# Optimization experiments

Hardware: AMD Instinct MI355X
Metric: run time of the kernel (lower is better)

Reference implementation:

```python
import jax, jax.numpy as jnp
import numpy as np

S = 256      # pair sequence length (multiple of 32 -> no padding needed)
C = 128      # pair hidden dim
H = 4        # n_heads
D = 32       # head_dim
EPS = 1e-5
ENDING = False


def setup_inputs() -> dict:
    key = jax.random.key(0)
    ks = jax.random.split(key, 10)
    s = 0.02
    return {
        "x": jax.random.normal(ks[0], (1, S, S, C), dtype=jnp.float32),
        "ln_w": jnp.ones((C,), dtype=jnp.float32),
        "ln_b": jnp.zeros((C,), dtype=jnp.float32),
        "w_bias": jax.random.normal(ks[1], (H, C), dtype=jnp.float32) * s,   # linear.weight
        "w_q": jax.random.normal(ks[2], (H * D, C), dtype=jnp.float32) * s,  # linear_q.weight
        "w_k": jax.random.normal(ks[3], (H * D, C), dtype=jnp.float32) * s,
        "w_v": jax.random.normal(ks[4], (H * D, C), dtype=jnp.float32) * s,
        "w_g": jax.random.normal(ks[5], (H * D, C), dtype=jnp.float32) * s,  # linear_g.weight
        "w_o": jax.random.normal(ks[6], (C, H * D), dtype=jnp.float32) * s,  # linear_o.weight
    }


def reference(x, ln_w, ln_b, w_bias, w_q, w_k, w_v, w_g, w_o):
    h = x[0]  # [S, S, C]
    if ENDING:
        h = jnp.transpose(h, (1, 0, 2))
    # LayerNorm over channel dim
    mu = jnp.mean(h, axis=-1, keepdims=True)
    var = jnp.mean(jnp.square(h - mu), axis=-1, keepdims=True)
    h = (h - mu) * jax.lax.rsqrt(var + EPS) * ln_w + ln_b

    # pair-derived additive bias: [H, S, S], broadcast over the row (batch) dim
    tri_bias = jnp.einsum("ijc,hc->hij", h, w_bias)

    # per-head Q/K/V: weights are [H*D, C] with head-major rows
    wq = w_q.reshape(H, D, C)
    wk = w_k.reshape(H, D, C)
    wv = w_v.reshape(H, D, C)
    q = jnp.einsum("ijc,hdc->hijd", h, wq)  # [H, S(row), S(seq), D]
    k = jnp.einsum("ijc,hdc->hijd", h, wk)
    v = jnp.einsum("ijc,hdc->hijd", h, wv)

    scale = D ** -0.5
    # scores[h, i, j, k] = scale * q[h,i,j]\cdot k[h,i,k] + bias[h, j, k]
    scores = jnp.einsum("hijd,hikd->hijk", q, k) * scale + tri_bias[:, None, :, :]
    attn = jax.nn.softmax(scores, axis=-1)
    o = jnp.einsum("hijk,hikd->hijd", attn, v)          # [H, S, S, D]
    o = jnp.transpose(o, (1, 2, 0, 3)).reshape(S, S, H * D)

    # sigmoid gating and output projection
    g = jax.nn.sigmoid(jnp.einsum("ijc,ec->ije", h, w_g))
    out = jnp.einsum("ije,ce->ijc", o * g, w_o)          # [S, S, C]
    if ENDING:
        out = jnp.transpose(out, (1, 0, 2))
    return out[None]  # [1, S, S, C]
```

## Files before the change

kernel.cpp:

```cpp
#include <hip/hip_runtime.h>
#include <hip/hip_bf16.h>
#include <math.h>

#define SS 256
#define CC 128
#define NH 4
#define HD 32
#define M_TOT (SS*SS)
#define HEAD_STRIDE (M_TOT*HD)
#define PSTR 72
#define SCALE 0.17677669529663687f
#define QSCL 0.25507602861154995f
#define LOG2E 1.4426950408889634f

typedef short short8 __attribute__((ext_vector_type(8)));
typedef float f32x4 __attribute__((ext_vector_type(4)));
typedef unsigned short ushort_t;

static __device__ __forceinline__ unsigned int f2bf(float f) {
  unsigned int u = __builtin_bit_cast(unsigned int, f);
  u += 0x7fffu + ((u >> 16) & 1u);
  return u >> 16;
}
static __device__ __forceinline__ float bf2f(unsigned short b) {
  unsigned int u = ((unsigned int)b) << 16;
  return __builtin_bit_cast(float, u);
}

static __device__ __forceinline__ void async_copy16(const void* g, void* l) {
  __builtin_amdgcn_global_load_lds(
      (const __attribute__((address_space(1))) unsigned int*)g,
      (__attribute__((address_space(3))) unsigned int*)l, 16, 0, 0);
}

__global__ __launch_bounds__(256) void pack_w(
    const float* __restrict__ wq, const float* __restrict__ wk,
    const float* __restrict__ wv, const float* __restrict__ wg,
    const float* __restrict__ wb, const float* __restrict__ wo,
    ushort_t* __restrict__ wcomb, ushort_t* __restrict__ wbias,
    ushort_t* __restrict__ wobf) {
  int idx = blockIdx.x*256 + threadIdx.x;
  if (idx >= 656*128) return;
  int n = idx >> 7, kk = idx & 127;
  if (n < 512) {
    float val;
    if (n < 128)      val = wq[n*128 + kk];
    else if (n < 256) val = wk[(n-128)*128 + kk];
    else if (n < 384) val = wv[(n-256)*128 + kk];
    else              val = wg[(n-384)*128 + kk];
    wcomb[idx] = (ushort_t)f2bf(val);
  } else if (n < 528) {
    int r = n - 512;
    wbias[r*128 + kk] = (r < NH) ? (ushort_t)f2bf(wb[r*128 + kk] * LOG2E) : (ushort_t)0;
  } else {
    int r = n - 528;
    wobf[r*128 + kk] = (ushort_t)f2bf(wo[r*128 + kk]);
  }
}

__global__ __launch_bounds__(256, 2) void fused_proj(
    const float* __restrict__ x, const float* __restrict__ ln_w,
    const float* __restrict__ ln_b, const ushort_t* __restrict__ wcomb,
    const ushort_t* __restrict__ wbias,
    ushort_t* __restrict__ qb, ushort_t* __restrict__ kb,
    ushort_t* __restrict__ vb, ushort_t* __restrict__ gbf,
    float* __restrict__ biasF) {
  __shared__ ushort_t Ash[128*128];
  __shared__ ushort_t Bsh[128*128];
  int mbase = blockIdx.x * 128;
  int tid = threadIdx.x;
  int wvi = tid >> 6, lane = tid & 63;
  int quad = lane >> 4, l15 = lane & 15;
  int lrow4 = lane >> 4;
  int cl = lane & 15;

  #pragma unroll
  for (int t = 0; t < 8; t++) {
    int inst = wvi*8 + t;
    int row = inst*4 + lrow4;
    int gc = cl ^ (row & 7);
    async_copy16(wcomb + (size_t)row*128 + gc*8, Bsh + inst*512);
  }

  {
    int l = tid & 31;
    int rsub = tid >> 5;
    float4 w4 = *(const float4*)&ln_w[l*4];
    float4 b4 = *(const float4*)&ln_b[l*4];
    const float* xb = x + (size_t)(mbase + rsub)*CC + l*4;
    float4 vv[16];
    #pragma unroll
    for (int pass = 0; pass < 16; pass++)
      vv[pass] = *(const float4*)(xb + (size_t)pass*8*CC);
    #pragma unroll
    for (int pass = 0; pass < 16; pass++) {
      int row = pass*8 + rsub;
      float4 v = vv[pass];
      float s  = v.x + v.y + v.z + v.w;
      float s2 = v.x*v.x + v.y*v.y + v.z*v.z + v.w*v.w;
      #pragma unroll
      for (int o = 16; o > 0; o >>= 1) {
        s  += __shfl_xor(s, o);
        s2 += __shfl_xor(s2, o);
      }
      float mu  = s * (1.0f/CC);
      float var = s2 * (1.0f/CC) - mu*mu;
      float r = rsqrtf(var + 1e-5f);
      ushort4 o4;
      o4.x = (ushort_t)f2bf((v.x - mu) * r * w4.x + b4.x);
      o4.y = (ushort_t)f2bf((v.y - mu) * r * w4.y + b4.y);
      o4.z = (ushort_t)f2bf((v.z - mu) * r * w4.z + b4.z);
      o4.w = (ushort_t)f2bf((v.w - mu) * r * w4.w + b4.w);
      int addr = row*128 + (((l >> 1) ^ (row & 7)) << 3) + (l & 1)*4;
      *(ushort4*)&Ash[addr] = o4;
    }
  }
  __syncthreads();

  int wrow = (wvi >> 1) * 64, wcol = (wvi & 1) * 64;
  const f32x4 fz = {0.f,0.f,0.f,0.f};

  short8 Afr[4][4];
  #pragma unroll
  for (int s = 0; s < 4; s++)
    #pragma unroll
    for (int f = 0; f < 4; f++) {
      int ra = wrow + f*16 + l15;
      Afr[s][f] = *(const short8*)&Ash[ra*128 + (((s*4+quad) ^ (ra&7)) << 3)];
    }

  #pragma unroll
  for (int sec = 0; sec < 4; sec++) {
    f32x4 acc[4][4];
    #pragma unroll
    for (int a = 0; a < 4; a++)
      #pragma unroll
      for (int b = 0; b < 4; b++) acc[a][b] = fz;

    #pragma unroll
    for (int s = 0; s < 4; s++) {
      short8 Bf[4];
      #pragma unroll
      for (int f = 0; f < 4; f++) {
        int rb = wcol + f*16 + l15;
        Bf[f] = *(const short8*)&Bsh[rb*128 + (((s*4+quad) ^ (rb&7)) << 3)];
      }
      #pragma unroll
      for (int mi = 0; mi < 4; mi++)
        #pragma unroll
        for (int ni = 0; ni < 4; ni++)
          acc[mi][ni] = __builtin_amdgcn_mfma_f32_16x16x32_bf16(Bf[ni], Afr[s][mi], acc[mi][ni], 0, 0, 0);
    }

    __syncthreads();

    if (sec < 3) {
      #pragma unroll
      for (int t = 0; t < 8; t++) {
        int inst = wvi*8 + t;
        int row = inst*4 + lrow4;
        int gc = cl ^ (row & 7);
        async_copy16(wcomb + (size_t)((sec+1)*128 + row)*128 + gc*8, Bsh + inst*512);
      }
    }

    #pragma unroll
    for (int mi = 0; mi < 4; mi++) {
      int m = mbase + wrow + mi*16 + l15;
      #pragma unroll
      for (int ni = 0; ni < 4; ni++) {
        int n = wcol + ni*16 + quad*4;
        f32x4 v4 = acc[mi][ni];
        if (sec == 0) {
          ushort4 o4;
          o4.x = (ushort_t)f2bf(v4[0] * QSCL);
          o4.y = (ushort_t)f2bf(v4[1] * QSCL);
          o4.z = (ushort_t)f2bf(v4[2] * QSCL);
          o4.w = (ushort_t)f2bf(v4[3] * QSCL);
          *(ushort4*)&qb[(size_t)(n>>5)*HEAD_STRIDE + (size_t)m*HD + (n&31)] = o4;
        } else if (sec == 1) {
          ushort4 o4;
          o4.x = (ushort_t)f2bf(v4[0]);
          o4.y = (ushort_t)f2bf(v4[1]);
          o4.z = (ushort_t)f2bf(v4[2]);
          o4.w = (ushort_t)f2bf(v4[3]);
          *(ushort4*)&kb[(size_t)(n>>5)*HEAD_STRIDE + (size_t)m*HD + (n&31)] = o4;
        } else if (sec == 2) {
          ushort4 o4;
          o4.x = (ushort_t)f2bf(v4[0]);
          o4.y = (ushort_t)f2bf(v4[1]);
          o4.z = (ushort_t)f2bf(v4[2]);
          o4.w = (ushort_t)f2bf(v4[3]);
          *(ushort4*)&vb[(size_t)(n>>5)*HEAD_STRIDE + (size_t)m*HD + (n&31)] = o4;
        } else {
          ushort4 o4;
          o4.x = (ushort_t)f2bf(1.0f/(1.0f + __expf(-v4[0])));
          o4.y = (ushort_t)f2bf(1.0f/(1.0f + __expf(-v4[1])));
          o4.z = (ushort_t)f2bf(1.0f/(1.0f + __expf(-v4[2])));
          o4.w = (ushort_t)f2bf(1.0f/(1.0f + __expf(-v4[3])));
          *(ushort4*)&gbf[(size_t)m*CC + n] = o4;
        }
      }
    }

    if (sec == 0) {
      short8 wbF[4];
      #pragma unroll
      for (int s = 0; s < 4; s++)
        wbF[s] = *(const short8*)&wbias[l15*128 + s*32 + quad*8];
      #pragma unroll
      for (int t2 = 0; t2 < 2; t2++) {
        int f2 = wvi*2 + t2;
        f32x4 bacc = fz;
        #pragma unroll
        for (int s = 0; s < 4; s++) {
          int ra = f2*16 + l15;
          short8 Af = *(const short8*)&Ash[ra*128 + (((s*4+quad) ^ (ra&7)) << 3)];
          bacc = __builtin_amdgcn_mfma_f32_16x16x32_bf16(wbF[s], Af, bacc, 0, 0, 0);
        }
        if (quad == 0) {
          int m = mbase + f2*16 + l15;
          int ji = m >> 8, ki = m & 255;
          int jt = ji >> 4, q2 = (ji >> 2) & 3, rg = ji & 3;
          int kt = ki >> 4, lf = ki & 15;
          #pragma unroll
          for (int r = 0; r < 4; r++)
            biasF[(size_t)(((r*16 + jt)*16 + kt) << 8) + (q2*16 + lf)*4 + rg] = bacc[r];
        }
      }
    }

    if (sec < 3) __syncthreads();
  }
}

__global__ __launch_bounds__(256, 3) void attn_mfma(
    const ushort_t* __restrict__ qb, const ushort_t* __restrict__ kb,
    const ushort_t* __restrict__ vb, const float* __restrict__ biasF,
    const ushort_t* __restrict__ gbf, ushort_t* __restrict__ ogated) {
  __shared__ ushort_t Vt[32*256];
  __shared__ ushort_t Pb[4*64*PSTR];
  int i = blockIdx.x, hh = blockIdx.y;
  int tid = threadIdx.x;
  int wvi = tid >> 6, lane = tid & 63;
  int quad = lane >> 4, l15 = lane & 15;

  {
    const ushort_t* vrow = vb + ((size_t)hh*M_TOT + (size_t)i*SS + tid) * HD;
    const uint4* v4 = (const uint4*)vrow;
    int cs = tid >> 3, ce = tid & 7;
    #pragma unroll
    for (int c = 0; c < 4; c++) {
      uint4 r = v4[c];
      unsigned int u[4] = {r.x, r.y, r.z, r.w};
      #pragma unroll
      for (int w = 0; w < 4; w++) {
        int d = c*8 + w*2;
        Vt[d*256     + ((cs ^ (d&7))     << 3) + ce] = (ushort_t)(u[w] & 0xffffu);
        Vt[(d+1)*256 + ((cs ^ ((d+1)&7)) << 3) + ce] = (ushort_t)(u[w] >> 16);
      }
    }
  }

  const ushort_t* qbase = qb + ((size_t)hh*M_TOT + (size_t)i*SS + wvi*64) * HD;
  short8 Qf[4];
  #pragma unroll
  for (int a = 0; a < 4; a++)
    Qf[a] = *(const short8*)(qbase + (a*16 + l15)*HD + quad*8);

  const ushort_t* kbp = kb + ((size_t)hh*M_TOT + (size_t)i*SS) * HD;
  const float* bb = biasF + (size_t)(hh*16 + wvi*4) * 4096;

  const f32x4 fz = {0.f, 0.f, 0.f, 0.f};
  f32x4 Oa[4][2];
  #pragma unroll
  for (int a = 0; a < 4; a++) { Oa[a][0] = fz; Oa[a][1] = fz; }
  float lsum[4][4] = {};

  ushort_t* pw = Pb + wvi*64*PSTR;

  __syncthreads();

  #pragma unroll
  for (int it = 0; it < 4; it++) {
    #pragma unroll
    for (int b = 0; b < 4; b++) {
      int kt = it*4 + b;
      short8 Kf = *(const short8*)(kbp + (kt*16 + l15)*HD + quad*8);
      #pragma unroll
      for (int a = 0; a < 4; a++) {
        float4 bt = *(const float4*)(bb + (size_t)((a*16 + kt) << 8) + lane*4);
        f32x4 bias4 = {bt.x, bt.y, bt.z, bt.w};
        f32x4 S = __builtin_amdgcn_mfma_f32_16x16x32_bf16(Qf[a], Kf, bias4, 0, 0, 0);
        float p0 = __builtin_amdgcn_exp2f(S[0]);
        float p1 = __builtin_amdgcn_exp2f(S[1]);
        float p2 = __builtin_amdgcn_exp2f(S[2]);
        float p3 = __builtin_amdgcn_exp2f(S[3]);
        lsum[a][0] += p0; lsum[a][1] += p1; lsum[a][2] += p2; lsum[a][3] += p3;
        ushort_t* pwa = pw + (a*16 + quad*4)*PSTR + b*16 + l15;
        pwa[0*PSTR] = (ushort_t)f2bf(p0);
        pwa[1*PSTR] = (ushort_t)f2bf(p1);
        pwa[2*PSTR] = (ushort_t)f2bf(p2);
        pwa[3*PSTR] = (ushort_t)f2bf(p3);
      }
    }
    #pragma unroll
    for (int kk = 0; kk < 2; kk++) {
      int cb = it*8 + kk*4;
      int sw = ((cb + quad) ^ (l15 & 7)) << 3;
      short8 Vf0 = *(const short8*)&Vt[l15*256 + sw];
      short8 Vf1 = *(const short8*)&Vt[(16 + l15)*256 + sw];
      #pragma unroll
      for (int a = 0; a < 4; a++) {
        short8 Pf = *(const short8*)&pw[(a*16 + l15)*PSTR + kk*32 + quad*8];
        Oa[a][0] = __builtin_amdgcn_mfma_f32_16x16x32_bf16(Pf, Vf0, Oa[a][0], 0, 0, 0);
        Oa[a][1] = __builtin_amdgcn_mfma_f32_16x16x32_bf16(Pf, Vf1, Oa[a][1], 0, 0, 0);
      }
    }
  }

  float linv[4][4];
  #pragma unroll
  for (int a = 0; a < 4; a++) {
    #pragma unroll
    for (int r = 0; r < 4; r++) {
      float v = lsum[a][r];
      v += __shfl_xor(v, 1);
      v += __shfl_xor(v, 2);
      v += __shfl_xor(v, 4);
      v += __shfl_xor(v, 8);
      linv[a][r] = 1.0f / v;
    }
  }
  const ushort_t* gp = gbf + ((size_t)i*SS + wvi*64)*CC + hh*HD;
  ushort_t* ob = ogated + ((size_t)i*SS + wvi*64)*CC + hh*HD;
  #pragma unroll
  for (int a = 0; a < 4; a++) {
    #pragma unroll
    for (int r = 0; r < 4; r++) {
      int row = (a*16 + quad*4 + r) * CC;
      float g0 = bf2f(gp[row + l15]);
      float g1 = bf2f(gp[row + 16 + l15]);
      ob[row + l15]      = (ushort_t)f2bf(Oa[a][0][r] * linv[a][r] * g0);
      ob[row + 16 + l15] = (ushort_t)f2bf(Oa[a][1][r] * linv[a][r] * g1);
    }
  }
}

__global__ __launch_bounds__(256, 3) void out_mfma(
    const ushort_t* __restrict__ ogated, const ushort_t* __restrict__ wobf,
    float* __restrict__ out) {
  __shared__ ushort_t Bsh[128*128];
  int mbase = blockIdx.x * 128;
  int tid = threadIdx.x;
  int wvi = tid >> 6, lane = tid & 63;
  int quad = lane >> 4, l15 = lane & 15;

  {
    int lrow4 = lane >> 4;
    int cl = lane & 15;
    #pragma unroll
    for (int t = 0; t < 8; t++) {
      int inst = wvi*8 + t;
      int row = inst*4 + lrow4;
      int gc = cl ^ (row & 7);
      async_copy16(wobf + (size_t)row*128 + gc*8, Bsh + inst*512);
    }
  }
  __syncthreads();

  int wrow = (wvi >> 1) * 64, wcol = (wvi & 1) * 64;
  const f32x4 fz = {0.f,0.f,0.f,0.f};
  f32x4 acc[4][4];
  #pragma unroll
  for (int a = 0; a < 4; a++)
    #pragma unroll
    for (int b = 0; b < 4; b++) acc[a][b] = fz;

  #pragma unroll
  for (int s = 0; s < 4; s++) {
    short8 Af[4], Bf[4];
    #pragma unroll
    for (int f = 0; f < 4; f++) {
      int ra = mbase + wrow + f*16 + l15;
      Af[f] = *(const short8*)&ogated[(size_t)ra*128 + s*32 + quad*8];
      int rb = wcol + f*16 + l15;
      Bf[f] = *(const short8*)&Bsh[rb*128 + (((s*4+quad) ^ (rb&7)) << 3)];
    }
    #pragma unroll
    for (int mi = 0; mi < 4; mi++)
      #pragma unroll
      for (int ni = 0; ni < 4; ni++)
        acc[mi][ni] = __builtin_amdgcn_mfma_f32_16x16x32_bf16(Bf[ni], Af[mi], acc[mi][ni], 0, 0, 0);
  }

  #pragma unroll
  for (int mi = 0; mi < 4; mi++) {
    int m = mbase + wrow + mi*16 + l15;
    #pragma unroll
    for (int ni = 0; ni < 4; ni++) {
      int n = wcol + ni*16 + quad*4;
      float4 st;
      st.x = acc[mi][ni][0];
      st.y = acc[mi][ni][1];
      st.z = acc[mi][ni][2];
      st.w = acc[mi][ni][3];
      *(float4*)&out[(size_t)m*CC + n] = st;
    }
  }
}

extern "C" void kernel_launch(void* const* d_in, const int* in_sizes, int n_in,
                              void* d_out, int out_size, void* d_ws, size_t ws_size,
                              hipStream_t stream) {
  const float* x    = (const float*)d_in[0];
  const float* ln_w = (const float*)d_in[1];
  const float* ln_b = (const float*)d_in[2];
  const float* w_bias = (const float*)d_in[3];
  const float* w_q  = (const float*)d_in[4];
  const float* w_k  = (const float*)d_in[5];
  const float* w_v  = (const float*)d_in[6];
  const float* w_g  = (const float*)d_in[7];
  const float* w_o  = (const float*)d_in[8];
  float* out = (float*)d_out;

  char* B = (char*)d_ws;
  ushort_t* ogated = (ushort_t*)(B + 0);
  ushort_t* qb    = (ushort_t*)(B + 16777216);
  ushort_t* kb    = (ushort_t*)(B + 33554432);
  ushort_t* vb    = (ushort_t*)(B + 50331648);
  ushort_t* gbf   = (ushort_t*)(B + 67108864);
  float*    biasF = (float*)   (B + 83886080);
  ushort_t* wcomb = (ushort_t*)(B + 84934656);
  ushort_t* wbias = (ushort_t*)(B + 85065728);
  ushort_t* wobf  = (ushort_t*)(B + 85069824);

  pack_w<<<(656*128 + 255)/256, 256, 0, stream>>>(w_q, w_k, w_v, w_g, w_bias, w_o,
                                                  wcomb, wbias, wobf);
  fused_proj<<<M_TOT/128, 256, 0, stream>>>(x, ln_w, ln_b, wcomb, wbias,
                                            qb, kb, vb, gbf, biasF);
  attn_mfma<<<dim3(SS, NH), 256, 0, stream>>>(qb, kb, vb, biasF, gbf, ogated);
  out_mfma<<<M_TOT/128, 256, 0, stream>>>(ogated, wobf, out);
}
```

Baseline: 162.7 us.

## Transpose attention MFMA outputs so P and O rows stay in-lane

Swaps the MFMA operand order for both the score and PV products so each lane holds four consecutive key or head-dim elements of a single query row. P can then be written to LDS as one packed 8-byte store instead of four strided scalar stores, and the row-sum reduction drops to two cross-lane shuffles. The bias tensor layout written by the projection kernel is permuted to match. P tiles shrink to 32 keys per step with a smaller padded stride, which frees LDS; occupancy is raised to 4 blocks, s_setprio is added around the PV MFMAs, and the gating epilogue uses vectorized loads and stores. The risks are more register pressure at the higher occupancy and more synchronisation-free steps per iteration.

```diff
diff --git a/kernel.cpp b/kernel.cpp
--- a/kernel.cpp
+++ b/kernel.cpp
@@ -8,7 +8,7 @@
 #define HD 32
 #define M_TOT (SS*SS)
 #define HEAD_STRIDE (M_TOT*HD)
-#define PSTR 72
+#define PSTR2 40
 #define SCALE 0.17677669529663687f
 #define QSCL 0.25507602861154995f
 #define LOG2E 1.4426950408889634f
@@ -221,11 +221,11 @@
         if (quad == 0) {
           int m = mbase + f2*16 + l15;
           int ji = m >> 8, ki = m & 255;
-          int jt = ji >> 4, q2 = (ji >> 2) & 3, rg = ji & 3;
-          int kt = ki >> 4, lf = ki & 15;
+          int jt = ji >> 4, lj = ji & 15;
+          int kt = ki >> 4, qk = (ki >> 2) & 3, rk = ki & 3;
           #pragma unroll
           for (int r = 0; r < 4; r++)
-            biasF[(size_t)(((r*16 + jt)*16 + kt) << 8) + (q2*16 + lf)*4 + rg] = bacc[r];
+            biasF[(size_t)(((r*16 + jt)*16 + kt) << 8) + (qk*16 + lj)*4 + rk] = bacc[r];
         }
       }
     }
@@ -234,12 +234,12 @@
   }
 }
 
-__global__ __launch_bounds__(256, 3) void attn_mfma(
+__global__ __launch_bounds__(256, 4) void attn_mfma(
     const ushort_t* __restrict__ qb, const ushort_t* __restrict__ kb,
     const ushort_t* __restrict__ vb, const float* __restrict__ biasF,
     const ushort_t* __restrict__ gbf, ushort_t* __restrict__ ogated) {
   __shared__ ushort_t Vt[32*256];
-  __shared__ ushort_t Pb[4*64*PSTR];
+  __shared__ ushort_t Pb[4*64*PSTR2];
   int i = blockIdx.x, hh = blockIdx.y;
   int tid = threadIdx.x;
   int wvi = tid >> 6, lane = tid & 63;
@@ -275,75 +275,76 @@
   f32x4 Oa[4][2];
   #pragma unroll
   for (int a = 0; a < 4; a++) { Oa[a][0] = fz; Oa[a][1] = fz; }
-  float lsum[4][4] = {};
-
-  ushort_t* pw = Pb + wvi*64*PSTR;
+  float lsum[4] = {0.f, 0.f, 0.f, 0.f};
+
+  ushort_t* pw = Pb + wvi*64*PSTR2;
 
   __syncthreads();
 
   #pragma unroll
-  for (int it = 0; it < 4; it++) {
-    #pragma unroll
-    for (int b = 0; b < 4; b++) {
-      int kt = it*4 + b;
+  for (int it = 0; it < 8; it++) {
+    #pragma unroll
+    for (int b = 0; b < 2; b++) {
+      int kt = it*2 + b;
       short8 Kf = *(const short8*)(kbp + (kt*16 + l15)*HD + quad*8);
       #pragma unroll
       for (int a = 0; a < 4; a++) {
         float4 bt = *(const float4*)(bb + (size_t)((a*16 + kt) << 8) + lane*4);
         f32x4 bias4 = {bt.x, bt.y, bt.z, bt.w};
-        f32x4 S = __builtin_amdgcn_mfma_f32_16x16x32_bf16(Qf[a], Kf, bias4, 0, 0, 0);
+        f32x4 S = __builtin_amdgcn_mfma_f32_16x16x32_bf16(Kf, Qf[a], bias4, 0, 0, 0);
         float p0 = __builtin_amdgcn_exp2f(S[0]);
         float p1 = __builtin_amdgcn_exp2f(S[1]);
         float p2 = __builtin_amdgcn_exp2f(S[2]);
         float p3 = __builtin_amdgcn_exp2f(S[3]);
-        lsum[a][0] += p0; lsum[a][1] += p1; lsum[a][2] += p2; lsum[a][3] += p3;
-        ushort_t* pwa = pw + (a*16 + quad*4)*PSTR + b*16 + l15;
-        pwa[0*PSTR] = (ushort_t)f2bf(p0);
-        pwa[1*PSTR] = (ushort_t)f2bf(p1);
-        pwa[2*PSTR] = (ushort_t)f2bf(p2);
-        pwa[3*PSTR] = (ushort_t)f2bf(p3);
-      }
-    }
-    #pragma unroll
-    for (int kk = 0; kk < 2; kk++) {
-      int cb = it*8 + kk*4;
-      int sw = ((cb + quad) ^ (l15 & 7)) << 3;
-      short8 Vf0 = *(const short8*)&Vt[l15*256 + sw];
-      short8 Vf1 = *(const short8*)&Vt[(16 + l15)*256 + sw];
-      #pragma unroll
-      for (int a = 0; a < 4; a++) {
-        short8 Pf = *(const short8*)&pw[(a*16 + l15)*PSTR + kk*32 + quad*8];
-        Oa[a][0] = __builtin_amdgcn_mfma_f32_16x16x32_bf16(Pf, Vf0, Oa[a][0], 0, 0, 0);
-        Oa[a][1] = __builtin_amdgcn_mfma_f32_16x16x32_bf16(Pf, Vf1, Oa[a][1], 0, 0, 0);
-      }
-    }
-  }
-
-  float linv[4][4];
+        lsum[a] += (p0 + p1) + (p2 + p3);
+        ushort4 o4;
+        o4.x = (ushort_t)f2bf(p0);
+        o4.y = (ushort_t)f2bf(p1);
+        o4.z = (ushort_t)f2bf(p2);
+        o4.w = (ushort_t)f2bf(p3);
+        *(ushort4*)&pw[(a*16 + l15)*PSTR2 + b*16 + quad*4] = o4;
+      }
+    }
+    int sw = ((it*4 + quad) ^ (l15 & 7)) << 3;
+    short8 Vf0 = *(const short8*)&Vt[l15*256 + sw];
+    short8 Vf1 = *(const short8*)&Vt[(16 + l15)*256 + sw];
+    __builtin_amdgcn_s_setprio(1);
+    #pragma unroll
+    for (int a = 0; a < 4; a++) {
+      short8 Pf = *(const short8*)&pw[(a*16 + l15)*PSTR2 + quad*8];
+      Oa[a][0] = __builtin_amdgcn_mfma_f32_16x16x32_bf16(Vf0, Pf, Oa[a][0], 0, 0, 0);
+      Oa[a][1] = __builtin_amdgcn_mfma_f32_16x16x32_bf16(Vf1, Pf, Oa[a][1], 0, 0, 0);
+    }
+    __builtin_amdgcn_s_setprio(0);
+  }
+
+  float linv[4];
   #pragma unroll
   for (int a = 0; a < 4; a++) {
-    #pragma unroll
-    for (int r = 0; r < 4; r++) {
-      float v = lsum[a][r];
-      v += __shfl_xor(v, 1);
-      v += __shfl_xor(v, 2);
-      v += __shfl_xor(v, 4);
-      v += __shfl_xor(v, 8);
-      linv[a][r] = 1.0f / v;
-    }
-  }
+    float v = lsum[a];
+    v += __shfl_xor(v, 16);
+    v += __shfl_xor(v, 32);
+    linv[a] = 1.0f / v;
+  }
+
   const ushort_t* gp = gbf + ((size_t)i*SS + wvi*64)*CC + hh*HD;
   ushort_t* ob = ogated + ((size_t)i*SS + wvi*64)*CC + hh*HD;
   #pragma unroll
   for (int a = 0; a < 4; a++) {
-    #pragma unroll
-    for (int r = 0; r < 4; r++) {
-      int row = (a*16 + quad*4 + r) * CC;
-      float g0 = bf2f(gp[row + l15]);
-      float g1 = bf2f(gp[row + 16 + l15]);
-      ob[row + l15]      = (ushort_t)f2bf(Oa[a][0][r] * linv[a][r] * g0);
-      ob[row + 16 + l15] = (ushort_t)f2bf(Oa[a][1][r] * linv[a][r] * g1);
-    }
+    int rowoff = (a*16 + l15)*CC;
+    ushort4 g0 = *(const ushort4*)&gp[rowoff + quad*4];
+    ushort4 g1 = *(const ushort4*)&gp[rowoff + 16 + quad*4];
+    ushort4 o0, o1;
+    o0.x = (ushort_t)f2bf(Oa[a][0][0] * linv[a] * bf2f(g0.x));
+    o0.y = (ushort_t)f2bf(Oa[a][0][1] * linv[a] * bf2f(g0.y));
+    o0.z = (ushort_t)f2bf(Oa[a][0][2] * linv[a] * bf2f(g0.z));
+    o0.w = (ushort_t)f2bf(Oa[a][0][3] * linv[a] * bf2f(g0.w));
+    o1.x = (ushort_t)f2bf(Oa[a][1][0] * linv[a] * bf2f(g1.x));
+    o1.y = (ushort_t)f2bf(Oa[a][1][1] * linv[a] * bf2f(g1.y));
+    o1.z = (ushort_t)f2bf(Oa[a][1][2] * linv[a] * bf2f(g1.z));
+    o1.w = (ushort_t)f2bf(Oa[a][1][3] * linv[a] * bf2f(g1.w));
+    *(ushort4*)&ob[rowoff + quad*4] = o0;
+    *(ushort4*)&ob[rowoff + 16 + quad*4] = o1;
   }
 }
 
```

Result: no change. 159.6 us (-1.9%).
